# Kernel tuning notes

Measured on AMD Instinct MI355X. Metric: run time of the kernel, lower is better.

The kernel has to match this reference:

```python
import jax, jax.numpy as jnp
import numpy as np

DIM = 100   # hardcoded in the original module (A_100.npy / target_100.npy)
BATCH = 131072
B_COEF = 1.0  # self.B in the original module


def setup_inputs() -> dict:
    key = jax.random.key(0)
    k1, k2, k3 = jax.random.split(key, 3)
    # state layout per system: [x (DIM), e_x (DIM), W_c (DIM), W_a (DIM)]
    state = jax.random.normal(k1, (BATCH, 4 * DIM), dtype=jnp.float32)
    A = jax.random.normal(k2, (DIM, DIM), dtype=jnp.float32) / np.sqrt(DIM)
    target = jax.random.normal(k3, (DIM,), dtype=jnp.float32)
    return {"state": state, "A": A, "target": target}


def reference(state, A, target):
    # Faithful, batched translation of CA_event.forward(t, state):
    #   x, e_x, W_a are slices of the flattened 4*DIM state; W_c is unused in forward.
    d = DIM
    x = state[:, :d]            # [B, d]
    e_x = state[:, d:2 * d]     # [B, d]
    W_a = state[:, 3 * d:4 * d]  # [B, d]

    u = W_a * (x + e_x - target[None, :])          # control signal
    s = x * x / (1.0 + x * x)                      # sigmoid-like saturation Y^2/(1+Y^2)
    dx = -B_COEF * x + s @ A.T + u * s             # [B, d]

    zeros = jnp.zeros_like(x)
    # derivative ordering matches the original output tuple: (dx, -dx, 0 for W_c, 0 for W_a)
    return jnp.concatenate([dx, -dx, zeros, zeros], axis=-1)
```

## Files before the change

### kernel.cpp

```cpp
#include <hip/hip_runtime.h>

#define DIMX 100
#define BATCH 131072
#define BUFW 108

typedef __bf16 bf16x8 __attribute__((ext_vector_type(8)));
typedef __bf16 bf16x4 __attribute__((ext_vector_type(4)));
typedef float  f32x4  __attribute__((ext_vector_type(4)));

__global__ void conv_A(const float* __restrict__ A, __bf16* __restrict__ ws) {
    int i = blockIdx.x * 256 + threadIdx.x;
    if (i < 112 * 128) {
        int j = i >> 7, k = i & 127;
        float v = (j < DIMX && k < DIMX) ? A[j * DIMX + k] : 0.0f;
        ws[i] = (__bf16)v;
    }
}

template <bool USE_WS>
__global__ __launch_bounds__(128) void ca_main(
    const float* __restrict__ state, const float* __restrict__ Amat,
    const __bf16* __restrict__ Bws, const float* __restrict__ target,
    float* __restrict__ out)
{
    __shared__ __align__(16) __bf16 buf[2][16 * BUFW];

    const int tid = threadIdx.x;
    const int wave = tid >> 6, lane = tid & 63;
    __bf16* __restrict__ wbuf = buf[wave];
    const long r0 = (long)blockIdx.x * 32 + wave * 16;

#pragma unroll
    for (int it = 0; it < 7; ++it) {
        int i = lane + it * 64;
        if (i < 400) {
            int row = i / 25, c4 = i - row * 25, j0 = c4 * 4;
            const float* rp = state + (r0 + row) * 400;
            f32x4 x = *reinterpret_cast<const f32x4*>(rp + j0);
            f32x4 e = *reinterpret_cast<const f32x4*>(rp + DIMX + j0);
            f32x4 w = *reinterpret_cast<const f32x4*>(rp + 3 * DIMX + j0);
            f32x4 t = *reinterpret_cast<const f32x4*>(target + j0);
            bf16x4 b;
#pragma unroll
            for (int q = 0; q < 4; ++q) {
                float u  = w[q] * (x[q] + e[q] - t[q]);
                float x2 = x[q] * x[q];
                float s  = x2 * __builtin_amdgcn_rcpf(1.0f + x2);
                b[q] = (__bf16)fmaf(u, s, -x[q]);
            }
            *reinterpret_cast<bf16x4*>(&wbuf[row * BUFW + j0]) = b;
        }
    }

    const int fr = lane & 15, h = lane >> 4;
    const float* sp = state + (r0 + fr) * 400;
    bf16x8 afrag[4];
#pragma unroll
    for (int kt = 0; kt < 4; ++kt) {
        int k0 = kt * 32 + h * 8;
        bf16x8 f = {};
        if (k0 < DIMX) {
            f32x4 xa = *reinterpret_cast<const f32x4*>(sp + k0);
            f32x4 xb = *reinterpret_cast<const f32x4*>(sp + k0 + 4);
#pragma unroll
            for (int e = 0; e < 8; ++e) {
                float x = (e < 4) ? xa[e] : xb[e - 4];
                float x2 = x * x;
                float s = x2 * __builtin_amdgcn_rcpf(1.0f + x2);
                f[e] = (k0 + e < DIMX) ? (__bf16)s : (__bf16)0.0f;
            }
        }
        afrag[kt] = f;
    }

#pragma unroll
    for (int n = 0; n < 7; ++n) {
        f32x4 acc = {0.f, 0.f, 0.f, 0.f};
#pragma unroll
        for (int kt = 0; kt < 4; ++kt) {
            bf16x8 bf;
            if constexpr (USE_WS) {
                bf = *reinterpret_cast<const bf16x8*>(
                    Bws + (n * 16 + fr) * 128 + kt * 32 + h * 8);
            } else {
                int jj = n * 16 + fr;
#pragma unroll
                for (int e = 0; e < 8; ++e) {
                    int k = kt * 32 + h * 8 + e;
                    float v = (jj < DIMX && k < DIMX) ? Amat[jj * DIMX + k] : 0.0f;
                    bf[e] = (__bf16)v;
                }
            }
            acc = __builtin_amdgcn_mfma_f32_16x16x32_bf16(afrag[kt], bf, acc, 0, 0, 0);
        }
        int j = n * 16 + fr;
        if (j < DIMX) {
#pragma unroll
            for (int q = 0; q < 4; ++q) {
                int idx = (h * 4 + q) * BUFW + j;
                wbuf[idx] = (__bf16)((float)wbuf[idx] + acc[q]);
            }
        }
    }

#pragma unroll
    for (int it = 0; it < 25; ++it) {
        int i = lane + it * 64;
        int row = i / 100, c4 = i - row * 100;
        f32x4 v;
        if (c4 < 25) {
            bf16x4 d = *reinterpret_cast<const bf16x4*>(&wbuf[row * BUFW + c4 * 4]);
            v = f32x4{(float)d[0], (float)d[1], (float)d[2], (float)d[3]};
        } else if (c4 < 50) {
            bf16x4 d = *reinterpret_cast<const bf16x4*>(&wbuf[row * BUFW + c4 * 4 - DIMX]);
            v = f32x4{-(float)d[0], -(float)d[1], -(float)d[2], -(float)d[3]};
        } else {
            v = f32x4{0.f, 0.f, 0.f, 0.f};
        }
        __builtin_nontemporal_store(v,
            reinterpret_cast<f32x4*>(&out[(r0 + row) * 400 + c4 * 4]));
    }
}

extern "C" void kernel_launch(void* const* d_in, const int* in_sizes, int n_in,
                              void* d_out, int out_size, void* d_ws, size_t ws_size,
                              hipStream_t stream) {
    const float* state  = (const float*)d_in[0];
    const float* Amat   = (const float*)d_in[1];
    const float* target = (const float*)d_in[2];
    float* out = (float*)d_out;
    (void)in_sizes; (void)n_in; (void)out_size;

    if (ws_size >= (size_t)(112 * 128 * sizeof(__bf16))) {
        conv_A<<<dim3(56), dim3(256), 0, stream>>>(Amat, (__bf16*)d_ws);
        ca_main<true><<<dim3(BATCH / 32), dim3(128), 0, stream>>>(
            state, Amat, (const __bf16*)d_ws, target, out);
    } else {
        ca_main<false><<<dim3(BATCH / 32), dim3(128), 0, stream>>>(
            state, Amat, nullptr, target, out);
    }
}
```

Baseline: 71.56 us.

## Swap MFMA operands so each lane owns a row and drop LDS staging

The MFMA operand order is swapped so A is the first operand and the sigmoid fragment the second. Each lane's accumulator then holds four consecutive output columns of its own row. The elementwise control term is computed in registers in the epilogue and written straight to global memory as fp32, removing the LDS bf16 buffer and the separate prologue pass. The zero halves are written in a separate coalesced loop. The row-per-lane stores and loads are less coalesced than before (16 rows per wave, each lane touching a different 1600-byte row), and the intermediate no longer rounds to bf16, which also improves precision.

```diff
diff --git a/kernel.cpp b/kernel.cpp
--- a/kernel.cpp
+++ b/kernel.cpp
@@ -2,10 +2,8 @@
 
 #define DIMX 100
 #define BATCH 131072
-#define BUFW 108
 
 typedef __bf16 bf16x8 __attribute__((ext_vector_type(8)));
-typedef __bf16 bf16x4 __attribute__((ext_vector_type(4)));
 typedef float  f32x4  __attribute__((ext_vector_type(4)));
 
 __global__ void conv_A(const float* __restrict__ A, __bf16* __restrict__ ws) {
@@ -23,45 +21,22 @@
     const __bf16* __restrict__ Bws, const float* __restrict__ target,
     float* __restrict__ out)
 {
-    __shared__ __align__(16) __bf16 buf[2][16 * BUFW];
-
     const int tid = threadIdx.x;
     const int wave = tid >> 6, lane = tid & 63;
-    __bf16* __restrict__ wbuf = buf[wave];
+    const int fr = lane & 15, h = lane >> 4;
     const long r0 = (long)blockIdx.x * 32 + wave * 16;
+    const long row = r0 + fr;
+    const float* rp = state + row * 400;
+    float* op = out + row * 400;
 
-#pragma unroll
-    for (int it = 0; it < 7; ++it) {
-        int i = lane + it * 64;
-        if (i < 400) {
-            int row = i / 25, c4 = i - row * 25, j0 = c4 * 4;
-            const float* rp = state + (r0 + row) * 400;
-            f32x4 x = *reinterpret_cast<const f32x4*>(rp + j0);
-            f32x4 e = *reinterpret_cast<const f32x4*>(rp + DIMX + j0);
-            f32x4 w = *reinterpret_cast<const f32x4*>(rp + 3 * DIMX + j0);
-            f32x4 t = *reinterpret_cast<const f32x4*>(target + j0);
-            bf16x4 b;
-#pragma unroll
-            for (int q = 0; q < 4; ++q) {
-                float u  = w[q] * (x[q] + e[q] - t[q]);
-                float x2 = x[q] * x[q];
-                float s  = x2 * __builtin_amdgcn_rcpf(1.0f + x2);
-                b[q] = (__bf16)fmaf(u, s, -x[q]);
-            }
-            *reinterpret_cast<bf16x4*>(&wbuf[row * BUFW + j0]) = b;
-        }
-    }
-
-    const int fr = lane & 15, h = lane >> 4;
-    const float* sp = state + (r0 + fr) * 400;
-    bf16x8 afrag[4];
+    bf16x8 sfrag[4];
 #pragma unroll
     for (int kt = 0; kt < 4; ++kt) {
         int k0 = kt * 32 + h * 8;
         bf16x8 f = {};
         if (k0 < DIMX) {
-            f32x4 xa = *reinterpret_cast<const f32x4*>(sp + k0);
-            f32x4 xb = *reinterpret_cast<const f32x4*>(sp + k0 + 4);
+            f32x4 xa = *reinterpret_cast<const f32x4*>(rp + k0);
+            f32x4 xb = *reinterpret_cast<const f32x4*>(rp + k0 + 4);
 #pragma unroll
             for (int e = 0; e < 8; ++e) {
                 float x = (e < 4) ? xa[e] : xb[e - 4];
@@ -70,7 +45,17 @@
                 f[e] = (k0 + e < DIMX) ? (__bf16)s : (__bf16)0.0f;
             }
         }
-        afrag[kt] = f;
+        sfrag[kt] = f;
+    }
+
+#pragma unroll
+    for (int it = 0; it < 13; ++it) {
+        int i = lane + it * 64;
+        if (i < 800) {
+            int r = i / 50, c4 = i - r * 50;
+            __builtin_nontemporal_store(f32x4{0.f, 0.f, 0.f, 0.f},
+                reinterpret_cast<f32x4*>(&out[(r0 + r) * 400 + 200 + c4 * 4]));
+        }
     }
 
 #pragma unroll
@@ -78,9 +63,9 @@
         f32x4 acc = {0.f, 0.f, 0.f, 0.f};
 #pragma unroll
         for (int kt = 0; kt < 4; ++kt) {
-            bf16x8 bf;
+            bf16x8 af;
             if constexpr (USE_WS) {
-                bf = *reinterpret_cast<const bf16x8*>(
+                af = *reinterpret_cast<const bf16x8*>(
                     Bws + (n * 16 + fr) * 128 + kt * 32 + h * 8);
             } else {
                 int jj = n * 16 + fr;
@@ -88,37 +73,29 @@
                 for (int e = 0; e < 8; ++e) {
                     int k = kt * 32 + h * 8 + e;
                     float v = (jj < DIMX && k < DIMX) ? Amat[jj * DIMX + k] : 0.0f;
-                    bf[e] = (__bf16)v;
+                    af[e] = (__bf16)v;
                 }
             }
-            acc = __builtin_amdgcn_mfma_f32_16x16x32_bf16(afrag[kt], bf, acc, 0, 0, 0);
+            acc = __builtin_amdgcn_mfma_f32_16x16x32_bf16(af, sfrag[kt], acc, 0, 0, 0);
         }
-        int j = n * 16 + fr;
-        if (j < DIMX) {
+        int j0 = n * 16 + h * 4;
+        if (j0 < DIMX) {
+            f32x4 x = *reinterpret_cast<const f32x4*>(rp + j0);
+            f32x4 e = *reinterpret_cast<const f32x4*>(rp + DIMX + j0);
+            f32x4 w = *reinterpret_cast<const f32x4*>(rp + 3 * DIMX + j0);
+            f32x4 t = *reinterpret_cast<const f32x4*>(target + j0);
+            f32x4 dx, ndx;
 #pragma unroll
             for (int q = 0; q < 4; ++q) {
-                int idx = (h * 4 + q) * BUFW + j;
-                wbuf[idx] = (__bf16)((float)wbuf[idx] + acc[q]);
+                float u  = w[q] * (x[q] + e[q] - t[q]);
+                float x2 = x[q] * x[q];
+                float s  = x2 * __builtin_amdgcn_rcpf(1.0f + x2);
+                float v  = acc[q] + fmaf(u, s, -x[q]);
+                dx[q] = v; ndx[q] = -v;
             }
+            __builtin_nontemporal_store(dx,  reinterpret_cast<f32x4*>(op + j0));
+            __builtin_nontemporal_store(ndx, reinterpret_cast<f32x4*>(op + DIMX + j0));
         }
-    }
-
-#pragma unroll
-    for (int it = 0; it < 25; ++it) {
-        int i = lane + it * 64;
-        int row = i / 100, c4 = i - row * 100;
-        f32x4 v;
-        if (c4 < 25) {
-            bf16x4 d = *reinterpret_cast<const bf16x4*>(&wbuf[row * BUFW + c4 * 4]);
-            v = f32x4{(float)d[0], (float)d[1], (float)d[2], (float)d[3]};
-        } else if (c4 < 50) {
-            bf16x4 d = *reinterpret_cast<const bf16x4*>(&wbuf[row * BUFW + c4 * 4 - DIMX]);
-            v = f32x4{-(float)d[0], -(float)d[1], -(float)d[2], -(float)d[3]};
-        } else {
-            v = f32x4{0.f, 0.f, 0.f, 0.f};
-        }
-        __builtin_nontemporal_store(v,
-            reinterpret_cast<f32x4*>(&out[(r0 + row) * 400 + c4 * 4]));
     }
 }
 
```

Measured after the change: 125.6 us. 1.75x slower.
